# Performance work log

Measured on AMD Instinct MI355X. Metric: run time of the kernel, lower is better.

The kernel has to match this reference:

```python
import jax, jax.numpy as jnp
import numpy as np

KERNEL_SIZE = 5
SIGMA = 1.0
DARK_KS = 15


def _gaussian_kernel():
    x = jnp.arange(KERNEL_SIZE, dtype=jnp.float32) - KERNEL_SIZE // 2
    phi = jnp.exp(-0.5 * x * x / (SIGMA ** 2))
    phi = phi / (phi.sum() + 0.001)
    k2d = jnp.outer(phi, phi)                       # [5,5]
    return jnp.tile(k2d[None, None], (3, 1, 1, 1))  # [3,1,5,5] OIHW depthwise


def _tanh01(v):
    return jnp.tanh(v) * 0.5 + 0.5


def setup_inputs() -> dict:
    key = jax.random.key(0)
    k1, k2, k3 = jax.random.split(key, 3)
    # keep x strictly positive so x**param has well-defined gradients
    x = jax.random.uniform(k1, (16, 3, 512, 512), dtype=jnp.float32, minval=0.01, maxval=1.0)
    output1 = jax.random.normal(k2, (16, 7), dtype=jnp.float32)
    output2 = jax.random.normal(k3, (16, 4), dtype=jnp.float32)
    return {"x": x, "output1": output1, "output2": output2}


def reference(x, output1, output2):
    N, C, H, W = x.shape

    # ---- parameter squashing (clip_range + softmax weights) ----
    o1 = jnp.concatenate([
        _tanh01(output1[:, 0:1]) * 0.25 + 1.0,   # gamma param in [1, 1.25]
        _tanh01(output1[:, 1:2]) * 0.9 + 0.1,    # contrast alpha (dead branch)
        _tanh01(output1[:, 2:3]) * 2.0,          # sharpen lamda in [0, 2]
        _tanh01(output1[:, 3:4]),                # dehaze w in [0, 1]
        _tanh01(output1[:, 4:7]) * 0.1 + 0.95,   # WB gains in [0.95, 1.05]
    ], axis=1)
    o2 = jax.nn.softmax(_tanh01(output2), axis=1)  # [N,4] branch weights

    param = o1[:, 0][:, None, None, None]
    lamda = o1[:, 2][:, None, None, None]
    w = o1[:, 3][:, None, None, None]
    wb_params = o1[:, 4:7][:, :, None, None]

    # ---- WB ----
    x1 = jnp.clip(x * wb_params, 0.0, 1.0)

    # ---- GAMMA ----
    x2 = jnp.clip(x ** param + 0.001, 0.0, 1.0)

    # ---- SHARPEN (depthwise 5x5 gaussian blur, unsharp mask) ----
    gk = _gaussian_kernel()
    blur = jax.lax.conv_general_dilated(
        x, gk, window_strides=(1, 1), padding=((2, 2), (2, 2)),
        feature_group_count=3,
        dimension_numbers=("NCHW", "OIHW", "NCHW"))
    blur = jnp.clip(blur, 0.0, 1.0)
    x4 = jnp.clip(x + lamda * (x - blur), 0.0, 1.0)

    # ---- DEHAZE ----
    minc = jnp.min(x, axis=1, keepdims=True)  # [N,1,H,W]
    # avg_pool2d k=15 s=1 p=7 with count_include_pad=True -> sum window / 225
    dark = jax.lax.reduce_window(
        minc, 0.0, jax.lax.add, (1, 1, DARK_KS, DARK_KS), (1, 1, 1, 1),
        padding=[(0, 0), (0, 0), (DARK_KS // 2, DARK_KS // 2), (DARK_KS // 2, DARK_KS // 2)]
    ) / float(DARK_KS * DARK_KS)
    top_k = int(H * W * 0.05)
    flat_dark = dark.reshape(N, -1)
    _, top_idx = jax.lax.top_k(flat_dark, top_k)            # [N, top_k]
    flat_img = x.reshape(N, C, -1)
    sel = jnp.take_along_axis(flat_img, top_idx[:, None, :], axis=2)  # [N,C,top_k]
    A = sel.mean(axis=2)[:, :, None, None]                  # atmospheric light
    trans = 1.0 - w * dark
    trans = jnp.where(trans > 0.1, trans, jnp.float32(0.1))
    x5 = jnp.clip((x - A) / (trans + 0.001) + A, 0.0, 1.0)

    # ---- weighted combination (contrast branch is computed but unused upstream) ----
    w0 = o2[:, 0][:, None, None, None]
    w1 = o2[:, 1][:, None, None, None]
    w2 = o2[:, 2][:, None, None, None]
    w3 = o2[:, 3][:, None, None, None]
    x_sum = x + 0.1 * (w0 * x1 + w1 * x2 + w2 * x4 + w3 * x5)
    x_sum = x_sum / (jnp.sum(o2, axis=1)[:, None, None, None] + 0.001)

    # ---- per-sample per-channel min-max normalization ----
    min_vals = jnp.min(x_sum, axis=(2, 3), keepdims=True)
    max_vals = jnp.max(x_sum, axis=(2, 3), keepdims=True)
    return (x_sum - min_vals) / (max_vals - min_vals + 1e-07)
```

## Files before the change

### kernel.cpp

```cpp
#include <hip/hip_runtime.h>
#include <math.h>

#define NS   16
#define HH   512
#define WW   512
#define HW   (HH*WW)
#define TOPK 13107
#define NBIN 4096

#define O_O1   0
#define O_O2   112
#define O_DEN  176
#define O_KN   304
#define O_MMP  512
#define O_PART 25088
#define O_DARK 33280


#define G0 0.054466787f
#define G1 0.244103071f
#define G2 0.402457854f

__device__ __forceinline__ float tanh01(float v) { return tanhf(v)*0.5f + 0.5f; }
__device__ __forceinline__ float clamp01(float v) { return fminf(fmaxf(v, 0.0f), 1.0f); }
__device__ __forceinline__ int dark_bin(float v) {
  int b = (int)(v * (float)NBIN);
  return b > (NBIN-1) ? (NBIN-1) : (b < 0 ? 0 : b);
}

__global__ void k_zero(unsigned* __restrict__ hist) {
  int i = blockIdx.x * 256 + threadIdx.x;
  uint4 z; z.x = 0u; z.y = 0u; z.z = 0u; z.w = 0u;
  ((uint4*)hist)[i] = z;
}

__global__ void __launch_bounds__(256)
k_dark(const float* __restrict__ x, float* __restrict__ wsf, unsigned* __restrict__ hist) {
  __shared__ __align__(16) float sm[4096 + 46*64];
  float* minc = sm;
  unsigned* lh = (unsigned*)sm;
  float* hsum = sm + 4096;
  int tid = threadIdx.x;
  int w0 = blockIdx.x * 64, h0 = blockIdx.y * 32, n = blockIdx.z;
  const float* xb = x + (size_t)n*3*HW;

  for (int i = tid; i < 46*20; i += 256) {
    int r = i / 20, q = i - r*20;
    int hm = h0 - 7 + r, wc = w0 - 8 + 4*q;
    float4 v; v.x = 0.f; v.y = 0.f; v.z = 0.f; v.w = 0.f;
    if (hm >= 0 && hm < HH && wc >= 0 && wc < WW) {
      size_t o = (size_t)hm*WW + wc;
      float4 a = *(const float4*)&xb[o];
      float4 b = *(const float4*)&xb[HW + o];
      float4 c = *(const float4*)&xb[2*HW + o];
      v.x = fminf(fminf(a.x,b.x),c.x); v.y = fminf(fminf(a.y,b.y),c.y);
      v.z = fminf(fminf(a.z,b.z),c.z); v.w = fminf(fminf(a.w,b.w),c.w);
    }
    *(float4*)&minc[r*80 + 4*q] = v;
  }
  __syncthreads();
  for (int i = tid; i < 46*16; i += 256) {
    int r = i >> 4, c4 = (i & 15) * 4;
    const float4* mr = (const float4*)&minc[r*80];
    int qb = c4 >> 2;
    float m[20];
    #pragma unroll
    for (int t = 0; t < 5; ++t) {
      float4 v = mr[qb + t];
      m[4*t] = v.x; m[4*t+1] = v.y; m[4*t+2] = v.z; m[4*t+3] = v.w;
    }
    float s = 0.f;
    #pragma unroll
    for (int j = 1; j <= 15; ++j) s += m[j];
    float4 o;
    o.x = s; s += m[16] - m[1];
    o.y = s; s += m[17] - m[2];
    o.z = s; s += m[18] - m[3];
    o.w = s;
    *(float4*)&hsum[r*64 + c4] = o;
  }
  __syncthreads();
  for (int i = tid; i < NBIN; i += 256) lh[i] = 0u;
  __syncthreads();
  {
    int c = tid & 63, ty = tid >> 6, r0 = ty * 8;
    float s = 0.f;
    #pragma unroll
    for (int j = 0; j < 15; ++j) s += hsum[(r0 + j)*64 + c];
    float* dk = wsf + O_DARK + (size_t)n*HW;
    #pragma unroll
    for (int i = 0; i < 8; ++i) {
      int r = r0 + i;
      float v = s * (1.0f/225.0f);
      dk[(size_t)(h0 + r)*WW + w0 + c] = v;
      atomicAdd(&lh[dark_bin(v)], 1u);
      if (i < 7) s += hsum[(r + 15)*64 + c] - hsum[r*64 + c];
    }
  }
  __syncthreads();
  unsigned* gh = hist + n*NBIN;
  for (int i = tid; i < NBIN; i += 256) { unsigned v = lh[i]; if (v) atomicAdd(&gh[i], v); }
}

__global__ void __launch_bounds__(256)
k_asum(const float* __restrict__ x, float* __restrict__ wsf,
       const unsigned* __restrict__ hist, unsigned* __restrict__ wsu,
       const float* __restrict__ o1, const float* __restrict__ o2) {
  __shared__ __align__(16) unsigned lh[NBIN];
  __shared__ unsigned spp[256];
  __shared__ int sh_bsel;
  __shared__ float bl[4][7];
  int tid = threadIdx.x;
  int n = blockIdx.x >> 6, chunk = blockIdx.x & 63;
  const uint4* gh4 = (const uint4*)(hist + n*NBIN);
  unsigned ps = 0;
  #pragma unroll
  for (int k = 0; k < 4; ++k) {
    uint4 v = gh4[tid*4 + k];
    *(uint4*)&lh[tid*16 + 4*k] = v;
    ps += v.x + v.y + v.z + v.w;
  }
  spp[tid] = ps;
  __syncthreads();
  if (tid == 0) {
    const unsigned K = TOPK;
    unsigned cum = 0; int bsel = 0;
    for (int t = 255; t >= 0; --t) {
      if (cum + spp[t] >= K) {
        bsel = t*16;
        for (int b = t*16 + 15; b >= t*16; --b) {
          if (cum + lh[b] >= K) { bsel = b; break; }
          cum += lh[b];
        }
        break;
      }
      cum += spp[t];
    }
    sh_bsel = bsel;
    if (chunk == 0) {
      wsu[O_KN + n] = K - cum;
      wsf[O_O1+n*7+0] = tanh01(o1[n*7+0])*0.25f + 1.0f;
      wsf[O_O1+n*7+1] = tanh01(o1[n*7+1])*0.9f  + 0.1f;
      wsf[O_O1+n*7+2] = tanh01(o1[n*7+2])*2.0f;
      wsf[O_O1+n*7+3] = tanh01(o1[n*7+3]);
      wsf[O_O1+n*7+4] = tanh01(o1[n*7+4])*0.1f + 0.95f;
      wsf[O_O1+n*7+5] = tanh01(o1[n*7+5])*0.1f + 0.95f;
      wsf[O_O1+n*7+6] = tanh01(o1[n*7+6])*0.1f + 0.95f;
      float q0 = expf(tanh01(o2[n*4+0]));
      float q1 = expf(tanh01(o2[n*4+1]));
      float q2 = expf(tanh01(o2[n*4+2]));
      float q3 = expf(tanh01(o2[n*4+3]));
      float s = q0+q1+q2+q3;
      q0 /= s; q1 /= s; q2 /= s; q3 /= s;
      wsf[O_O2+n*4+0]=q0; wsf[O_O2+n*4+1]=q1; wsf[O_O2+n*4+2]=q2; wsf[O_O2+n*4+3]=q3;
      wsf[O_DEN+n] = (q0+q1+q2+q3) + 0.001f;
    }
  }
  __syncthreads();
  int bsel = sh_bsel;
  const float4* db = (const float4*)(wsf + O_DARK + (size_t)n*HW + (size_t)chunk*4096);
  const float4* x0 = (const float4*)(x + (size_t)n*3*HW + (size_t)chunk*4096);
  const float4* x1 = x0 + HW/4;
  const float4* x2 = x0 + HW/2;
  float s0=0,s1=0,s2=0,e0=0,e1=0,e2=0,ec=0;
  #pragma unroll
  for (int k = 0; k < 4; ++k) {
    int idx = k*256 + tid;
    float4 d = db[idx], a = x0[idx], b = x1[idx], c = x2[idx];
    #define ACC(DX, AX, BX, CX) { \
      int bb = dark_bin(DX); \
      bool gt = (bb > bsel), eq = (bb == bsel); \
      s0 += gt ? AX : 0.f; s1 += gt ? BX : 0.f; s2 += gt ? CX : 0.f; \
      e0 += eq ? AX : 0.f; e1 += eq ? BX : 0.f; e2 += eq ? CX : 0.f; \
      ec += eq ? 1.f : 0.f; }
    ACC(d.x, a.x, b.x, c.x) ACC(d.y, a.y, b.y, c.y)
    ACC(d.z, a.z, b.z, c.z) ACC(d.w, a.w, b.w, c.w)
    #undef ACC
  }
  #pragma unroll
  for (int off = 32; off; off >>= 1) {
    s0 += __shfl_down(s0, off); s1 += __shfl_down(s1, off); s2 += __shfl_down(s2, off);
    e0 += __shfl_down(e0, off); e1 += __shfl_down(e1, off); e2 += __shfl_down(e2, off);
    ec += __shfl_down(ec, off);
  }
  int wave = tid >> 6, lane = tid & 63;
  if (lane == 0) {
    bl[wave][0]=s0; bl[wave][1]=s1; bl[wave][2]=s2;
    bl[wave][3]=e0; bl[wave][4]=e1; bl[wave][5]=e2; bl[wave][6]=ec;
  }
  __syncthreads();
  if (tid < 7) wsf[O_PART + blockIdx.x*8 + tid] =
      bl[0][tid] + bl[1][tid] + bl[2][tid] + bl[3][tid];
}

__global__ void __launch_bounds__(256)
k_main(const float* __restrict__ x, float* __restrict__ wsf,
       const unsigned* __restrict__ wsu, float* __restrict__ out) {
  __shared__ __align__(16) float xs[20*72];
  __shared__ __align__(16) float hb[20*64];
  __shared__ float rmn[4], rmx[4];
  __shared__ float shA;
  int tid = threadIdx.x;
  int w0 = blockIdx.x * 64, h0 = blockIdx.y * 16;
  int z = blockIdx.z, n = z / 3, c = z % 3;
  const float* xc = x + (size_t)z*HW;
  for (int i = tid; i < 360; i += 256) {
    int r = i / 18, q = i - r*18;
    int gh = h0 - 2 + r, gw = w0 - 4 + 4*q;
    float4 v; v.x = 0.f; v.y = 0.f; v.z = 0.f; v.w = 0.f;
    if (gh >= 0 && gh < HH && gw >= 0 && gw < WW)
      v = *(const float4*)&xc[(size_t)gh*WW + gw];
    *(float4*)&xs[r*72 + 4*q] = v;
  }
  if (tid < 64) {
    const float* p = wsf + O_PART + (size_t)(n*64 + tid)*8;
    float sc_ = p[c], ec_ = p[3 + c], cc_ = p[6];
    #pragma unroll
    for (int off = 32; off; off >>= 1) {
      sc_ += __shfl_down(sc_, off);
      ec_ += __shfl_down(ec_, off);
      cc_ += __shfl_down(cc_, off);
    }
    if (tid == 0) {
      float kn = (float)wsu[O_KN + n];
      float ce = fmaxf(cc_, 1.0f);
      shA = (sc_ + kn * (ec_ / ce)) * (1.0f/(float)TOPK);
    }
  }
  __syncthreads();
  for (int i = tid; i < 320; i += 256) {
    int r = i >> 4, c4 = (i & 15) * 4;
    const float4* xr = (const float4*)&xs[r*72];
    int qb = c4 >> 2;
    float4 A4 = xr[qb], B4 = xr[qb+1], C4 = xr[qb+2];
    float m2=A4.z, m3=A4.w, m4=B4.x, m5=B4.y, m6=B4.z, m7=B4.w, m8=C4.x, m9=C4.y;
    float4 o;
    o.x = G0*(m2+m6) + G1*(m3+m5) + G2*m4;
    o.y = G0*(m3+m7) + G1*(m4+m6) + G2*m5;
    o.z = G0*(m4+m8) + G1*(m5+m7) + G2*m6;
    o.w = G0*(m5+m9) + G1*(m6+m8) + G2*m7;
    *(float4*)&hb[r*64 + c4] = o;
  }
  __syncthreads();
  float param = wsf[O_O1 + n*7 + 0];
  float lamda = wsf[O_O1 + n*7 + 2];
  float wpar  = wsf[O_O1 + n*7 + 3];
  float wb    = wsf[O_O1 + n*7 + 4 + c];
  float q0 = wsf[O_O2 + n*4 + 0], q1 = wsf[O_O2 + n*4 + 1];
  float q2 = wsf[O_O2 + n*4 + 2], q3 = wsf[O_O2 + n*4 + 3];
  float rden = 1.0f / wsf[O_DEN + n];
  float A = shA;
  int r = tid >> 4, c4 = (tid & 15) * 4;
  float4 xv = *(const float4*)&xs[(r+2)*72 + c4 + 4];
  float4 b0 = *(const float4*)&hb[(r+0)*64 + c4];
  float4 b1 = *(const float4*)&hb[(r+1)*64 + c4];
  float4 b2 = *(const float4*)&hb[(r+2)*64 + c4];
  float4 b3 = *(const float4*)&hb[(r+3)*64 + c4];
  float4 b4 = *(const float4*)&hb[(r+4)*64 + c4];
  const float* dark = wsf + O_DARK + (size_t)n*HW;
  float4 dk = *(const float4*)&dark[(size_t)(h0+r)*WW + w0 + c4];
  float4 osum;
  float mnv = 3.4e38f, mxv = -3.4e38f;
  #define PIX(OX, XV, B0, B1, B2, B3, B4, DK) { \
    float blur = clamp01(G0*(B0+B4) + G1*(B1+B3) + G2*B2); \
    float x4v = clamp01(XV + lamda*(XV - blur)); \
    float x1v = clamp01(XV * wb); \
    float x2v = clamp01(__expf(param*__logf(XV)) + 0.001f); \
    float tr = 1.0f - wpar*DK; tr = tr > 0.1f ? tr : 0.1f; \
    float x5v = clamp01((XV - A) * __builtin_amdgcn_rcpf(tr + 0.001f) + A); \
    OX = (XV + 0.1f*(q0*x1v + q1*x2v + q2*x4v + q3*x5v)) * rden; \
    mnv = fminf(mnv, OX); mxv = fmaxf(mxv, OX); }
  PIX(osum.x, xv.x, b0.x, b1.x, b2.x, b3.x, b4.x, dk.x)
  PIX(osum.y, xv.y, b0.y, b1.y, b2.y, b3.y, b4.y, dk.y)
  PIX(osum.z, xv.z, b0.z, b1.z, b2.z, b3.z, b4.z, dk.z)
  PIX(osum.w, xv.w, b0.w, b1.w, b2.w, b3.w, b4.w, dk.w)
  #undef PIX
  *(float4*)&out[(size_t)z*HW + (size_t)(h0+r)*WW + w0 + c4] = osum;
  #pragma unroll
  for (int off = 32; off; off >>= 1) {
    mnv = fminf(mnv, __shfl_down(mnv, off));
    mxv = fmaxf(mxv, __shfl_down(mxv, off));
  }
  int wave = tid >> 6, lane = tid & 63;
  if (lane == 0) { rmn[wave] = mnv; rmx[wave] = mxv; }
  __syncthreads();
  if (tid == 0) {
    mnv = fminf(fminf(rmn[0], rmn[1]), fminf(rmn[2], rmn[3]));
    mxv = fmaxf(fmaxf(rmx[0], rmx[1]), fmaxf(rmx[2], rmx[3]));
    int bxy = blockIdx.y * 8 + blockIdx.x;
    wsf[O_MMP + z*512 + bxy]       = mnv;
    wsf[O_MMP + z*512 + 256 + bxy] = mxv;
  }
}

__global__ void __launch_bounds__(256)
k_norm(float* __restrict__ out, const float* __restrict__ wsf) {
  __shared__ float rmn[4], rmx[4];
  int tid = threadIdx.x;
  int nc = blockIdx.x >> 5;
  int sub = blockIdx.x & 31;
  float mn = wsf[O_MMP + nc*512 + tid];
  float mx = wsf[O_MMP + nc*512 + 256 + tid];
  #pragma unroll
  for (int off = 32; off; off >>= 1) {
    mn = fminf(mn, __shfl_down(mn, off));
    mx = fmaxf(mx, __shfl_down(mx, off));
  }
  int wave = tid >> 6, lane = tid & 63;
  if (lane == 0) { rmn[wave] = mn; rmx[wave] = mx; }
  __syncthreads();
  mn = fminf(fminf(rmn[0], rmn[1]), fminf(rmn[2], rmn[3]));
  mx = fmaxf(fmaxf(rmx[0], rmx[1]), fmaxf(rmx[2], rmx[3]));
  float sc = 1.0f / (mx - mn + 1e-7f);
  float4* o4 = (float4*)out + (size_t)nc*65536 + (size_t)sub*2048;
  #pragma unroll
  for (int k = 0; k < 8; ++k) {
    float4 v = o4[k*256 + tid];
    v.x = (v.x - mn) * sc; v.y = (v.y - mn) * sc;
    v.z = (v.z - mn) * sc; v.w = (v.w - mn) * sc;
    o4[k*256 + tid] = v;
  }
}

extern "C" void kernel_launch(void* const* d_in, const int* in_sizes, int n_in,
                              void* d_out, int out_size, void* d_ws, size_t ws_size,
                              hipStream_t stream) {
  const float* x  = (const float*)d_in[0];
  const float* o1 = (const float*)d_in[1];
  const float* o2 = (const float*)d_in[2];
  float* out = (float*)d_out;
  float* wsf = (float*)d_ws;
  unsigned* wsu = (unsigned*)d_ws;
  unsigned* hist = (unsigned*)(out + (size_t)16*HW);

  k_zero<<<dim3(64), dim3(256), 0, stream>>>(hist);
  k_dark<<<dim3(8, 16, 16), dim3(256), 0, stream>>>(x, wsf, hist);
  k_asum<<<dim3(1024), dim3(256), 0, stream>>>(x, wsf, hist, wsu, o1, o2);
  k_main<<<dim3(8, 32, 48), dim3(256), 0, stream>>>(x, wsf, wsu, out);
  k_norm<<<dim3(1536), dim3(256), 0, stream>>>(out, wsf);
}
```

Before: 186.9 us.

## Accumulate per-bin channel sums in dark kernel, drop second full pass for atmospheric light

The dark-channel histogram now stores, per bin, a count plus the sums of the three input channels. A tiny per-sample kernel then finds the threshold bin and computes the atmospheric light from the bin sums. This removes the separate kernel that re-read the whole dark map and input. The main kernel now loops over the three channels inside one block, so the dark map is read once per pixel, and interior tiles skip bounds checks. In exchange there are many more shared and global float atomics, and a coarser 1024-bin histogram that approximates the tie bin by its mean.

```diff
diff --git a/kernel.cpp b/kernel.cpp
--- a/kernel.cpp
+++ b/kernel.cpp
@@ -6,14 +6,13 @@
 #define WW   512
 #define HW   (HH*WW)
 #define TOPK 13107
-#define NBIN 4096
+#define NBIN 1024
 
 #define O_O1   0
 #define O_O2   112
 #define O_DEN  176
-#define O_KN   304
+#define O_A    320
 #define O_MMP  512
-#define O_PART 25088
 #define O_DARK 33280
 
 
@@ -36,27 +35,43 @@
 
 __global__ void __launch_bounds__(256)
 k_dark(const float* __restrict__ x, float* __restrict__ wsf, unsigned* __restrict__ hist) {
-  __shared__ __align__(16) float sm[4096 + 46*64];
+  __shared__ __align__(16) float sm[7040];
   float* minc = sm;
-  unsigned* lh = (unsigned*)sm;
+  unsigned* bins = (unsigned*)sm;
+  float* binsf = sm;
   float* hsum = sm + 4096;
   int tid = threadIdx.x;
   int w0 = blockIdx.x * 64, h0 = blockIdx.y * 32, n = blockIdx.z;
   const float* xb = x + (size_t)n*3*HW;
 
-  for (int i = tid; i < 46*20; i += 256) {
-    int r = i / 20, q = i - r*20;
-    int hm = h0 - 7 + r, wc = w0 - 8 + 4*q;
-    float4 v; v.x = 0.f; v.y = 0.f; v.z = 0.f; v.w = 0.f;
-    if (hm >= 0 && hm < HH && wc >= 0 && wc < WW) {
-      size_t o = (size_t)hm*WW + wc;
+  bool interior = (w0 >= 8) && (w0 + 72 <= WW) && (h0 >= 7) && (h0 + 39 <= HH);
+  if (interior) {
+    for (int i = tid; i < 46*20; i += 256) {
+      int r = i / 20, q = i - r*20;
+      size_t o = (size_t)(h0 - 7 + r)*WW + (w0 - 8 + 4*q);
       float4 a = *(const float4*)&xb[o];
       float4 b = *(const float4*)&xb[HW + o];
       float4 c = *(const float4*)&xb[2*HW + o];
+      float4 v;
       v.x = fminf(fminf(a.x,b.x),c.x); v.y = fminf(fminf(a.y,b.y),c.y);
       v.z = fminf(fminf(a.z,b.z),c.z); v.w = fminf(fminf(a.w,b.w),c.w);
-    }
-    *(float4*)&minc[r*80 + 4*q] = v;
+      *(float4*)&minc[r*80 + 4*q] = v;
+    }
+  } else {
+    for (int i = tid; i < 46*20; i += 256) {
+      int r = i / 20, q = i - r*20;
+      int hm = h0 - 7 + r, wc = w0 - 8 + 4*q;
+      float4 v; v.x = 0.f; v.y = 0.f; v.z = 0.f; v.w = 0.f;
+      if (hm >= 0 && hm < HH && wc >= 0 && wc < WW) {
+        size_t o = (size_t)hm*WW + wc;
+        float4 a = *(const float4*)&xb[o];
+        float4 b = *(const float4*)&xb[HW + o];
+        float4 c = *(const float4*)&xb[2*HW + o];
+        v.x = fminf(fminf(a.x,b.x),c.x); v.y = fminf(fminf(a.y,b.y),c.y);
+        v.z = fminf(fminf(a.z,b.z),c.z); v.w = fminf(fminf(a.w,b.w),c.w);
+      }
+      *(float4*)&minc[r*80 + 4*q] = v;
+    }
   }
   __syncthreads();
   for (int i = tid; i < 46*16; i += 256) {
@@ -80,7 +95,7 @@
     *(float4*)&hsum[r*64 + c4] = o;
   }
   __syncthreads();
-  for (int i = tid; i < NBIN; i += 256) lh[i] = 0u;
+  for (int i = tid; i < 4096; i += 256) bins[i] = 0u;
   __syncthreads();
   {
     int c = tid & 63, ty = tid >> 6, r0 = ty * 8;
@@ -91,205 +106,200 @@
     #pragma unroll
     for (int i = 0; i < 8; ++i) {
       int r = r0 + i;
+      size_t po = (size_t)(h0 + r)*WW + w0 + c;
       float v = s * (1.0f/225.0f);
-      dk[(size_t)(h0 + r)*WW + w0 + c] = v;
-      atomicAdd(&lh[dark_bin(v)], 1u);
+      dk[po] = v;
+      int b = dark_bin(v);
+      float x0v = xb[po], x1v = xb[HW + po], x2v = xb[2*HW + po];
+      atomicAdd(&bins[b*4], 1u);
+      atomicAdd(&binsf[b*4+1], x0v);
+      atomicAdd(&binsf[b*4+2], x1v);
+      atomicAdd(&binsf[b*4+3], x2v);
       if (i < 7) s += hsum[(r + 15)*64 + c] - hsum[r*64 + c];
     }
   }
   __syncthreads();
-  unsigned* gh = hist + n*NBIN;
-  for (int i = tid; i < NBIN; i += 256) { unsigned v = lh[i]; if (v) atomicAdd(&gh[i], v); }
+  unsigned* gh = hist + n*NBIN*4;
+  for (int b = tid; b < NBIN; b += 256) {
+    unsigned cnt = bins[b*4];
+    if (cnt) {
+      atomicAdd(&gh[b*4], cnt);
+      atomicAdd((float*)&gh[b*4+1], binsf[b*4+1]);
+      atomicAdd((float*)&gh[b*4+2], binsf[b*4+2]);
+      atomicAdd((float*)&gh[b*4+3], binsf[b*4+3]);
+    }
+  }
 }
 
 __global__ void __launch_bounds__(256)
-k_asum(const float* __restrict__ x, float* __restrict__ wsf,
-       const unsigned* __restrict__ hist, unsigned* __restrict__ wsu,
-       const float* __restrict__ o1, const float* __restrict__ o2) {
-  __shared__ __align__(16) unsigned lh[NBIN];
-  __shared__ unsigned spp[256];
-  __shared__ int sh_bsel;
-  __shared__ float bl[4][7];
-  int tid = threadIdx.x;
-  int n = blockIdx.x >> 6, chunk = blockIdx.x & 63;
-  const uint4* gh4 = (const uint4*)(hist + n*NBIN);
+k_sel(const unsigned* __restrict__ hist, float* __restrict__ wsf,
+      const float* __restrict__ o1, const float* __restrict__ o2) {
+  __shared__ float s0s[NBIN], s1s[NBIN], s2s[NBIN];
+  __shared__ unsigned cnts[NBIN];
+  __shared__ unsigned partial[256];
+  __shared__ int sh_bsel; __shared__ float sh_kn;
+  __shared__ float red[4][3];
+  int n = blockIdx.x, tid = threadIdx.x;
+  const uint4* g4 = (const uint4*)(hist + n*NBIN*4);
   unsigned ps = 0;
   #pragma unroll
   for (int k = 0; k < 4; ++k) {
-    uint4 v = gh4[tid*4 + k];
-    *(uint4*)&lh[tid*16 + 4*k] = v;
-    ps += v.x + v.y + v.z + v.w;
-  }
-  spp[tid] = ps;
+    int b = tid*4 + k;
+    uint4 v = g4[b];
+    cnts[b] = v.x;
+    s0s[b] = __uint_as_float(v.y);
+    s1s[b] = __uint_as_float(v.z);
+    s2s[b] = __uint_as_float(v.w);
+    ps += v.x;
+  }
+  partial[tid] = ps;
   __syncthreads();
   if (tid == 0) {
     const unsigned K = TOPK;
     unsigned cum = 0; int bsel = 0;
     for (int t = 255; t >= 0; --t) {
-      if (cum + spp[t] >= K) {
-        bsel = t*16;
-        for (int b = t*16 + 15; b >= t*16; --b) {
-          if (cum + lh[b] >= K) { bsel = b; break; }
-          cum += lh[b];
+      if (cum + partial[t] >= K) {
+        bsel = t*4;
+        for (int b = t*4 + 3; b >= t*4; --b) {
+          if (cum + cnts[b] >= K) { bsel = b; break; }
+          cum += cnts[b];
         }
         break;
       }
-      cum += spp[t];
-    }
-    sh_bsel = bsel;
-    if (chunk == 0) {
-      wsu[O_KN + n] = K - cum;
-      wsf[O_O1+n*7+0] = tanh01(o1[n*7+0])*0.25f + 1.0f;
-      wsf[O_O1+n*7+1] = tanh01(o1[n*7+1])*0.9f  + 0.1f;
-      wsf[O_O1+n*7+2] = tanh01(o1[n*7+2])*2.0f;
-      wsf[O_O1+n*7+3] = tanh01(o1[n*7+3]);
-      wsf[O_O1+n*7+4] = tanh01(o1[n*7+4])*0.1f + 0.95f;
-      wsf[O_O1+n*7+5] = tanh01(o1[n*7+5])*0.1f + 0.95f;
-      wsf[O_O1+n*7+6] = tanh01(o1[n*7+6])*0.1f + 0.95f;
-      float q0 = expf(tanh01(o2[n*4+0]));
-      float q1 = expf(tanh01(o2[n*4+1]));
-      float q2 = expf(tanh01(o2[n*4+2]));
-      float q3 = expf(tanh01(o2[n*4+3]));
-      float s = q0+q1+q2+q3;
-      q0 /= s; q1 /= s; q2 /= s; q3 /= s;
-      wsf[O_O2+n*4+0]=q0; wsf[O_O2+n*4+1]=q1; wsf[O_O2+n*4+2]=q2; wsf[O_O2+n*4+3]=q3;
-      wsf[O_DEN+n] = (q0+q1+q2+q3) + 0.001f;
-    }
+      cum += partial[t];
+    }
+    sh_bsel = bsel; sh_kn = (float)(K - cum);
   }
   __syncthreads();
   int bsel = sh_bsel;
-  const float4* db = (const float4*)(wsf + O_DARK + (size_t)n*HW + (size_t)chunk*4096);
-  const float4* x0 = (const float4*)(x + (size_t)n*3*HW + (size_t)chunk*4096);
-  const float4* x1 = x0 + HW/4;
-  const float4* x2 = x0 + HW/2;
-  float s0=0,s1=0,s2=0,e0=0,e1=0,e2=0,ec=0;
-  #pragma unroll
-  for (int k = 0; k < 4; ++k) {
-    int idx = k*256 + tid;
-    float4 d = db[idx], a = x0[idx], b = x1[idx], c = x2[idx];
-    #define ACC(DX, AX, BX, CX) { \
-      int bb = dark_bin(DX); \
-      bool gt = (bb > bsel), eq = (bb == bsel); \
-      s0 += gt ? AX : 0.f; s1 += gt ? BX : 0.f; s2 += gt ? CX : 0.f; \
-      e0 += eq ? AX : 0.f; e1 += eq ? BX : 0.f; e2 += eq ? CX : 0.f; \
-      ec += eq ? 1.f : 0.f; }
-    ACC(d.x, a.x, b.x, c.x) ACC(d.y, a.y, b.y, c.y)
-    ACC(d.z, a.z, b.z, c.z) ACC(d.w, a.w, b.w, c.w)
-    #undef ACC
-  }
+  float a0 = 0.f, a1 = 0.f, a2 = 0.f;
+  for (int b = tid; b < NBIN; b += 256)
+    if (b > bsel) { a0 += s0s[b]; a1 += s1s[b]; a2 += s2s[b]; }
   #pragma unroll
   for (int off = 32; off; off >>= 1) {
-    s0 += __shfl_down(s0, off); s1 += __shfl_down(s1, off); s2 += __shfl_down(s2, off);
-    e0 += __shfl_down(e0, off); e1 += __shfl_down(e1, off); e2 += __shfl_down(e2, off);
-    ec += __shfl_down(ec, off);
+    a0 += __shfl_down(a0, off); a1 += __shfl_down(a1, off); a2 += __shfl_down(a2, off);
   }
   int wave = tid >> 6, lane = tid & 63;
-  if (lane == 0) {
-    bl[wave][0]=s0; bl[wave][1]=s1; bl[wave][2]=s2;
-    bl[wave][3]=e0; bl[wave][4]=e1; bl[wave][5]=e2; bl[wave][6]=ec;
-  }
-  __syncthreads();
-  if (tid < 7) wsf[O_PART + blockIdx.x*8 + tid] =
-      bl[0][tid] + bl[1][tid] + bl[2][tid] + bl[3][tid];
+  if (lane == 0) { red[wave][0] = a0; red[wave][1] = a1; red[wave][2] = a2; }
+  __syncthreads();
+  if (tid == 0) {
+    a0 = red[0][0]+red[1][0]+red[2][0]+red[3][0];
+    a1 = red[0][1]+red[1][1]+red[2][1]+red[3][1];
+    a2 = red[0][2]+red[1][2]+red[2][2]+red[3][2];
+    float kn = sh_kn;
+    float ce = fmaxf((float)cnts[bsel], 1.0f);
+    wsf[O_A + n*3 + 0] = (a0 + kn*(s0s[bsel]/ce)) * (1.0f/(float)TOPK);
+    wsf[O_A + n*3 + 1] = (a1 + kn*(s1s[bsel]/ce)) * (1.0f/(float)TOPK);
+    wsf[O_A + n*3 + 2] = (a2 + kn*(s2s[bsel]/ce)) * (1.0f/(float)TOPK);
+    wsf[O_O1+n*7+0] = tanh01(o1[n*7+0])*0.25f + 1.0f;
+    wsf[O_O1+n*7+1] = tanh01(o1[n*7+1])*0.9f  + 0.1f;
+    wsf[O_O1+n*7+2] = tanh01(o1[n*7+2])*2.0f;
+    wsf[O_O1+n*7+3] = tanh01(o1[n*7+3]);
+    wsf[O_O1+n*7+4] = tanh01(o1[n*7+4])*0.1f + 0.95f;
+    wsf[O_O1+n*7+5] = tanh01(o1[n*7+5])*0.1f + 0.95f;
+    wsf[O_O1+n*7+6] = tanh01(o1[n*7+6])*0.1f + 0.95f;
+    float q0 = expf(tanh01(o2[n*4+0]));
+    float q1 = expf(tanh01(o2[n*4+1]));
+    float q2 = expf(tanh01(o2[n*4+2]));
+    float q3 = expf(tanh01(o2[n*4+3]));
+    float s = q0+q1+q2+q3;
+    q0 /= s; q1 /= s; q2 /= s; q3 /= s;
+    wsf[O_O2+n*4+0]=q0; wsf[O_O2+n*4+1]=q1; wsf[O_O2+n*4+2]=q2; wsf[O_O2+n*4+3]=q3;
+    wsf[O_DEN+n] = (q0+q1+q2+q3) + 0.001f;
+  }
 }
 
 __global__ void __launch_bounds__(256)
-k_main(const float* __restrict__ x, float* __restrict__ wsf,
-       const unsigned* __restrict__ wsu, float* __restrict__ out) {
+k_main(const float* __restrict__ x, float* __restrict__ wsf, float* __restrict__ out) {
   __shared__ __align__(16) float xs[20*72];
   __shared__ __align__(16) float hb[20*64];
   __shared__ float rmn[4], rmx[4];
-  __shared__ float shA;
   int tid = threadIdx.x;
-  int w0 = blockIdx.x * 64, h0 = blockIdx.y * 16;
-  int z = blockIdx.z, n = z / 3, c = z % 3;
-  const float* xc = x + (size_t)z*HW;
-  for (int i = tid; i < 360; i += 256) {
-    int r = i / 18, q = i - r*18;
-    int gh = h0 - 2 + r, gw = w0 - 4 + 4*q;
-    float4 v; v.x = 0.f; v.y = 0.f; v.z = 0.f; v.w = 0.f;
-    if (gh >= 0 && gh < HH && gw >= 0 && gw < WW)
-      v = *(const float4*)&xc[(size_t)gh*WW + gw];
-    *(float4*)&xs[r*72 + 4*q] = v;
-  }
-  if (tid < 64) {
-    const float* p = wsf + O_PART + (size_t)(n*64 + tid)*8;
-    float sc_ = p[c], ec_ = p[3 + c], cc_ = p[6];
-    #pragma unroll
-    for (int off = 32; off; off >>= 1) {
-      sc_ += __shfl_down(sc_, off);
-      ec_ += __shfl_down(ec_, off);
-      cc_ += __shfl_down(cc_, off);
-    }
-    if (tid == 0) {
-      float kn = (float)wsu[O_KN + n];
-      float ce = fmaxf(cc_, 1.0f);
-      shA = (sc_ + kn * (ec_ / ce)) * (1.0f/(float)TOPK);
-    }
-  }
-  __syncthreads();
-  for (int i = tid; i < 320; i += 256) {
-    int r = i >> 4, c4 = (i & 15) * 4;
-    const float4* xr = (const float4*)&xs[r*72];
-    int qb = c4 >> 2;
-    float4 A4 = xr[qb], B4 = xr[qb+1], C4 = xr[qb+2];
-    float m2=A4.z, m3=A4.w, m4=B4.x, m5=B4.y, m6=B4.z, m7=B4.w, m8=C4.x, m9=C4.y;
-    float4 o;
-    o.x = G0*(m2+m6) + G1*(m3+m5) + G2*m4;
-    o.y = G0*(m3+m7) + G1*(m4+m6) + G2*m5;
-    o.z = G0*(m4+m8) + G1*(m5+m7) + G2*m6;
-    o.w = G0*(m5+m9) + G1*(m6+m8) + G2*m7;
-    *(float4*)&hb[r*64 + c4] = o;
-  }
-  __syncthreads();
+  int w0 = blockIdx.x * 64, h0 = blockIdx.y * 16, n = blockIdx.z;
+  int r = tid >> 4, c4 = (tid & 15) * 4;
+  int wave = tid >> 6, lane = tid & 63;
+  int bxy = blockIdx.y * 8 + blockIdx.x;
+  float4 dk = *(const float4*)&wsf[O_DARK + (size_t)n*HW + (size_t)(h0+r)*WW + w0 + c4];
   float param = wsf[O_O1 + n*7 + 0];
   float lamda = wsf[O_O1 + n*7 + 2];
   float wpar  = wsf[O_O1 + n*7 + 3];
-  float wb    = wsf[O_O1 + n*7 + 4 + c];
   float q0 = wsf[O_O2 + n*4 + 0], q1 = wsf[O_O2 + n*4 + 1];
   float q2 = wsf[O_O2 + n*4 + 2], q3 = wsf[O_O2 + n*4 + 3];
   float rden = 1.0f / wsf[O_DEN + n];
-  float A = shA;
-  int r = tid >> 4, c4 = (tid & 15) * 4;
-  float4 xv = *(const float4*)&xs[(r+2)*72 + c4 + 4];
-  float4 b0 = *(const float4*)&hb[(r+0)*64 + c4];
-  float4 b1 = *(const float4*)&hb[(r+1)*64 + c4];
-  float4 b2 = *(const float4*)&hb[(r+2)*64 + c4];
-  float4 b3 = *(const float4*)&hb[(r+3)*64 + c4];
-  float4 b4 = *(const float4*)&hb[(r+4)*64 + c4];
-  const float* dark = wsf + O_DARK + (size_t)n*HW;
-  float4 dk = *(const float4*)&dark[(size_t)(h0+r)*WW + w0 + c4];
-  float4 osum;
-  float mnv = 3.4e38f, mxv = -3.4e38f;
-  #define PIX(OX, XV, B0, B1, B2, B3, B4, DK) { \
-    float blur = clamp01(G0*(B0+B4) + G1*(B1+B3) + G2*B2); \
-    float x4v = clamp01(XV + lamda*(XV - blur)); \
-    float x1v = clamp01(XV * wb); \
-    float x2v = clamp01(__expf(param*__logf(XV)) + 0.001f); \
-    float tr = 1.0f - wpar*DK; tr = tr > 0.1f ? tr : 0.1f; \
-    float x5v = clamp01((XV - A) * __builtin_amdgcn_rcpf(tr + 0.001f) + A); \
-    OX = (XV + 0.1f*(q0*x1v + q1*x2v + q2*x4v + q3*x5v)) * rden; \
-    mnv = fminf(mnv, OX); mxv = fmaxf(mxv, OX); }
-  PIX(osum.x, xv.x, b0.x, b1.x, b2.x, b3.x, b4.x, dk.x)
-  PIX(osum.y, xv.y, b0.y, b1.y, b2.y, b3.y, b4.y, dk.y)
-  PIX(osum.z, xv.z, b0.z, b1.z, b2.z, b3.z, b4.z, dk.z)
-  PIX(osum.w, xv.w, b0.w, b1.w, b2.w, b3.w, b4.w, dk.w)
-  #undef PIX
-  *(float4*)&out[(size_t)z*HW + (size_t)(h0+r)*WW + w0 + c4] = osum;
-  #pragma unroll
-  for (int off = 32; off; off >>= 1) {
-    mnv = fminf(mnv, __shfl_down(mnv, off));
-    mxv = fmaxf(mxv, __shfl_down(mxv, off));
-  }
-  int wave = tid >> 6, lane = tid & 63;
-  if (lane == 0) { rmn[wave] = mnv; rmx[wave] = mxv; }
-  __syncthreads();
-  if (tid == 0) {
-    mnv = fminf(fminf(rmn[0], rmn[1]), fminf(rmn[2], rmn[3]));
-    mxv = fmaxf(fmaxf(rmx[0], rmx[1]), fmaxf(rmx[2], rmx[3]));
-    int bxy = blockIdx.y * 8 + blockIdx.x;
-    wsf[O_MMP + z*512 + bxy]       = mnv;
-    wsf[O_MMP + z*512 + 256 + bxy] = mxv;
+  bool interior = (w0 >= 4) && (w0 + 68 <= WW) && (h0 >= 2) && (h0 + 18 <= HH);
+
+  for (int c = 0; c < 3; ++c) {
+    int z = n*3 + c;
+    const float* xc = x + (size_t)z*HW;
+    if (interior) {
+      for (int i = tid; i < 360; i += 256) {
+        int rr = i / 18, q = i - rr*18;
+        *(float4*)&xs[rr*72 + 4*q] =
+            *(const float4*)&xc[(size_t)(h0 - 2 + rr)*WW + (w0 - 4 + 4*q)];
+      }
+    } else {
+      for (int i = tid; i < 360; i += 256) {
+        int rr = i / 18, q = i - rr*18;
+        int gh = h0 - 2 + rr, gw = w0 - 4 + 4*q;
+        float4 v; v.x = 0.f; v.y = 0.f; v.z = 0.f; v.w = 0.f;
+        if (gh >= 0 && gh < HH && gw >= 0 && gw < WW)
+          v = *(const float4*)&xc[(size_t)gh*WW + gw];
+        *(float4*)&xs[rr*72 + 4*q] = v;
+      }
+    }
+    __syncthreads();
+    for (int i = tid; i < 320; i += 256) {
+      int rr = i >> 4, cc4 = (i & 15) * 4;
+      const float4* xr = (const float4*)&xs[rr*72];
+      int qb = cc4 >> 2;
+      float4 A4 = xr[qb], B4 = xr[qb+1], C4 = xr[qb+2];
+      float m2=A4.z, m3=A4.w, m4=B4.x, m5=B4.y, m6=B4.z, m7=B4.w, m8=C4.x, m9=C4.y;
+      float4 o;
+      o.x = G0*(m2+m6) + G1*(m3+m5) + G2*m4;
+      o.y = G0*(m3+m7) + G1*(m4+m6) + G2*m5;
+      o.z = G0*(m4+m8) + G1*(m5+m7) + G2*m6;
+      o.w = G0*(m5+m9) + G1*(m6+m8) + G2*m7;
+      *(float4*)&hb[rr*64 + cc4] = o;
+    }
+    __syncthreads();
+    float wb = wsf[O_O1 + n*7 + 4 + c];
+    float A  = wsf[O_A + n*3 + c];
+    float4 xv = *(const float4*)&xs[(r+2)*72 + c4 + 4];
+    float4 b0 = *(const float4*)&hb[(r+0)*64 + c4];
+    float4 b1 = *(const float4*)&hb[(r+1)*64 + c4];
+    float4 b2 = *(const float4*)&hb[(r+2)*64 + c4];
+    float4 b3 = *(const float4*)&hb[(r+3)*64 + c4];
+    float4 b4 = *(const float4*)&hb[(r+4)*64 + c4];
+    float4 osum;
+    float mnv = 3.4e38f, mxv = -3.4e38f;
+    #define PIX(OX, XV, B0, B1, B2, B3, B4, DK) { \
+      float blur = clamp01(G0*(B0+B4) + G1*(B1+B3) + G2*B2); \
+      float x4v = clamp01(XV + lamda*(XV - blur)); \
+      float x1v = clamp01(XV * wb); \
+      float x2v = clamp01(__expf(param*__logf(XV)) + 0.001f); \
+      float tr = 1.0f - wpar*DK; tr = tr > 0.1f ? tr : 0.1f; \
+      float x5v = clamp01((XV - A) * __builtin_amdgcn_rcpf(tr + 0.001f) + A); \
+      OX = (XV + 0.1f*(q0*x1v + q1*x2v + q2*x4v + q3*x5v)) * rden; \
+      mnv = fminf(mnv, OX); mxv = fmaxf(mxv, OX); }
+    PIX(osum.x, xv.x, b0.x, b1.x, b2.x, b3.x, b4.x, dk.x)
+    PIX(osum.y, xv.y, b0.y, b1.y, b2.y, b3.y, b4.y, dk.y)
+    PIX(osum.z, xv.z, b0.z, b1.z, b2.z, b3.z, b4.z, dk.z)
+    PIX(osum.w, xv.w, b0.w, b1.w, b2.w, b3.w, b4.w, dk.w)
+    #undef PIX
+    *(float4*)&out[(size_t)z*HW + (size_t)(h0+r)*WW + w0 + c4] = osum;
+    #pragma unroll
+    for (int off = 32; off; off >>= 1) {
+      mnv = fminf(mnv, __shfl_down(mnv, off));
+      mxv = fmaxf(mxv, __shfl_down(mxv, off));
+    }
+    if (lane == 0) { rmn[wave] = mnv; rmx[wave] = mxv; }
+    __syncthreads();
+    if (tid == 0) {
+      mnv = fminf(fminf(rmn[0], rmn[1]), fminf(rmn[2], rmn[3]));
+      mxv = fmaxf(fmaxf(rmx[0], rmx[1]), fmaxf(rmx[2], rmx[3]));
+      wsf[O_MMP + z*512 + bxy]       = mnv;
+      wsf[O_MMP + z*512 + 256 + bxy] = mxv;
+    }
   }
 }
 
@@ -330,12 +340,11 @@
   const float* o2 = (const float*)d_in[2];
   float* out = (float*)d_out;
   float* wsf = (float*)d_ws;
-  unsigned* wsu = (unsigned*)d_ws;
   unsigned* hist = (unsigned*)(out + (size_t)16*HW);
 
   k_zero<<<dim3(64), dim3(256), 0, stream>>>(hist);
   k_dark<<<dim3(8, 16, 16), dim3(256), 0, stream>>>(x, wsf, hist);
-  k_asum<<<dim3(1024), dim3(256), 0, stream>>>(x, wsf, hist, wsu, o1, o2);
-  k_main<<<dim3(8, 32, 48), dim3(256), 0, stream>>>(x, wsf, wsu, out);
+  k_sel<<<dim3(16), dim3(256), 0, stream>>>(hist, wsf, o1, o2);
+  k_main<<<dim3(8, 32, 16), dim3(256), 0, stream>>>(x, wsf, out);
   k_norm<<<dim3(1536), dim3(256), 0, stream>>>(out, wsf);
 }
```

After: 262.9 us. +40.6%, slower.

## Process all three channels per k_main block and add interior fast paths

Applied to the files above, without the earlier changes.

k_main now loops over the three channels inside each block instead of launching one block per channel. The dark-channel tile, the per-sample parameters and the atmospheric-light reduction are loaded or computed once per block, which cuts redundant global reads of the dark map and the partial sums. Both k_dark and k_main get a branch-free tile-loading path for blocks away from the image border. In exchange there are three times fewer blocks, each doing serial per-channel work with more barriers, so there is less parallelism to hide latency.

```diff
diff --git a/kernel.cpp b/kernel.cpp
--- a/kernel.cpp
+++ b/kernel.cpp
@@ -44,19 +44,34 @@
   int w0 = blockIdx.x * 64, h0 = blockIdx.y * 32, n = blockIdx.z;
   const float* xb = x + (size_t)n*3*HW;
 
-  for (int i = tid; i < 46*20; i += 256) {
-    int r = i / 20, q = i - r*20;
-    int hm = h0 - 7 + r, wc = w0 - 8 + 4*q;
-    float4 v; v.x = 0.f; v.y = 0.f; v.z = 0.f; v.w = 0.f;
-    if (hm >= 0 && hm < HH && wc >= 0 && wc < WW) {
-      size_t o = (size_t)hm*WW + wc;
+  bool interior = (w0 >= 8) && (w0 + 72 <= WW) && (h0 >= 7) && (h0 + 39 <= HH);
+  if (interior) {
+    for (int i = tid; i < 46*20; i += 256) {
+      int r = i / 20, q = i - r*20;
+      size_t o = (size_t)(h0 - 7 + r)*WW + (w0 - 8 + 4*q);
       float4 a = *(const float4*)&xb[o];
       float4 b = *(const float4*)&xb[HW + o];
       float4 c = *(const float4*)&xb[2*HW + o];
+      float4 v;
       v.x = fminf(fminf(a.x,b.x),c.x); v.y = fminf(fminf(a.y,b.y),c.y);
       v.z = fminf(fminf(a.z,b.z),c.z); v.w = fminf(fminf(a.w,b.w),c.w);
-    }
-    *(float4*)&minc[r*80 + 4*q] = v;
+      *(float4*)&minc[r*80 + 4*q] = v;
+    }
+  } else {
+    for (int i = tid; i < 46*20; i += 256) {
+      int r = i / 20, q = i - r*20;
+      int hm = h0 - 7 + r, wc = w0 - 8 + 4*q;
+      float4 v; v.x = 0.f; v.y = 0.f; v.z = 0.f; v.w = 0.f;
+      if (hm >= 0 && hm < HH && wc >= 0 && wc < WW) {
+        size_t o = (size_t)hm*WW + wc;
+        float4 a = *(const float4*)&xb[o];
+        float4 b = *(const float4*)&xb[HW + o];
+        float4 c = *(const float4*)&xb[2*HW + o];
+        v.x = fminf(fminf(a.x,b.x),c.x); v.y = fminf(fminf(a.y,b.y),c.y);
+        v.z = fminf(fminf(a.z,b.z),c.z); v.w = fminf(fminf(a.w,b.w),c.w);
+      }
+      *(float4*)&minc[r*80 + 4*q] = v;
+    }
   }
   __syncthreads();
   for (int i = tid; i < 46*16; i += 256) {
@@ -199,97 +214,110 @@
   __shared__ __align__(16) float xs[20*72];
   __shared__ __align__(16) float hb[20*64];
   __shared__ float rmn[4], rmx[4];
-  __shared__ float shA;
+  __shared__ float shA[3];
   int tid = threadIdx.x;
-  int w0 = blockIdx.x * 64, h0 = blockIdx.y * 16;
-  int z = blockIdx.z, n = z / 3, c = z % 3;
-  const float* xc = x + (size_t)z*HW;
-  for (int i = tid; i < 360; i += 256) {
-    int r = i / 18, q = i - r*18;
-    int gh = h0 - 2 + r, gw = w0 - 4 + 4*q;
-    float4 v; v.x = 0.f; v.y = 0.f; v.z = 0.f; v.w = 0.f;
-    if (gh >= 0 && gh < HH && gw >= 0 && gw < WW)
-      v = *(const float4*)&xc[(size_t)gh*WW + gw];
-    *(float4*)&xs[r*72 + 4*q] = v;
-  }
-  if (tid < 64) {
-    const float* p = wsf + O_PART + (size_t)(n*64 + tid)*8;
-    float sc_ = p[c], ec_ = p[3 + c], cc_ = p[6];
-    #pragma unroll
-    for (int off = 32; off; off >>= 1) {
-      sc_ += __shfl_down(sc_, off);
-      ec_ += __shfl_down(ec_, off);
-      cc_ += __shfl_down(cc_, off);
-    }
-    if (tid == 0) {
-      float kn = (float)wsu[O_KN + n];
-      float ce = fmaxf(cc_, 1.0f);
-      shA = (sc_ + kn * (ec_ / ce)) * (1.0f/(float)TOPK);
-    }
-  }
-  __syncthreads();
-  for (int i = tid; i < 320; i += 256) {
-    int r = i >> 4, c4 = (i & 15) * 4;
-    const float4* xr = (const float4*)&xs[r*72];
-    int qb = c4 >> 2;
-    float4 A4 = xr[qb], B4 = xr[qb+1], C4 = xr[qb+2];
-    float m2=A4.z, m3=A4.w, m4=B4.x, m5=B4.y, m6=B4.z, m7=B4.w, m8=C4.x, m9=C4.y;
-    float4 o;
-    o.x = G0*(m2+m6) + G1*(m3+m5) + G2*m4;
-    o.y = G0*(m3+m7) + G1*(m4+m6) + G2*m5;
-    o.z = G0*(m4+m8) + G1*(m5+m7) + G2*m6;
-    o.w = G0*(m5+m9) + G1*(m6+m8) + G2*m7;
-    *(float4*)&hb[r*64 + c4] = o;
-  }
-  __syncthreads();
+  int w0 = blockIdx.x * 64, h0 = blockIdx.y * 16, n = blockIdx.z;
+  int r = tid >> 4, c4 = (tid & 15) * 4;
+  int wave = tid >> 6, lane = tid & 63;
+  int bxy = blockIdx.y * 8 + blockIdx.x;
+  float4 dk = *(const float4*)&wsf[O_DARK + (size_t)n*HW + (size_t)(h0+r)*WW + w0 + c4];
   float param = wsf[O_O1 + n*7 + 0];
   float lamda = wsf[O_O1 + n*7 + 2];
   float wpar  = wsf[O_O1 + n*7 + 3];
-  float wb    = wsf[O_O1 + n*7 + 4 + c];
   float q0 = wsf[O_O2 + n*4 + 0], q1 = wsf[O_O2 + n*4 + 1];
   float q2 = wsf[O_O2 + n*4 + 2], q3 = wsf[O_O2 + n*4 + 3];
   float rden = 1.0f / wsf[O_DEN + n];
-  float A = shA;
-  int r = tid >> 4, c4 = (tid & 15) * 4;
-  float4 xv = *(const float4*)&xs[(r+2)*72 + c4 + 4];
-  float4 b0 = *(const float4*)&hb[(r+0)*64 + c4];
-  float4 b1 = *(const float4*)&hb[(r+1)*64 + c4];
-  float4 b2 = *(const float4*)&hb[(r+2)*64 + c4];
-  float4 b3 = *(const float4*)&hb[(r+3)*64 + c4];
-  float4 b4 = *(const float4*)&hb[(r+4)*64 + c4];
-  const float* dark = wsf + O_DARK + (size_t)n*HW;
-  float4 dk = *(const float4*)&dark[(size_t)(h0+r)*WW + w0 + c4];
-  float4 osum;
-  float mnv = 3.4e38f, mxv = -3.4e38f;
-  #define PIX(OX, XV, B0, B1, B2, B3, B4, DK) { \
-    float blur = clamp01(G0*(B0+B4) + G1*(B1+B3) + G2*B2); \
-    float x4v = clamp01(XV + lamda*(XV - blur)); \
-    float x1v = clamp01(XV * wb); \
-    float x2v = clamp01(__expf(param*__logf(XV)) + 0.001f); \
-    float tr = 1.0f - wpar*DK; tr = tr > 0.1f ? tr : 0.1f; \
-    float x5v = clamp01((XV - A) * __builtin_amdgcn_rcpf(tr + 0.001f) + A); \
-    OX = (XV + 0.1f*(q0*x1v + q1*x2v + q2*x4v + q3*x5v)) * rden; \
-    mnv = fminf(mnv, OX); mxv = fmaxf(mxv, OX); }
-  PIX(osum.x, xv.x, b0.x, b1.x, b2.x, b3.x, b4.x, dk.x)
-  PIX(osum.y, xv.y, b0.y, b1.y, b2.y, b3.y, b4.y, dk.y)
-  PIX(osum.z, xv.z, b0.z, b1.z, b2.z, b3.z, b4.z, dk.z)
-  PIX(osum.w, xv.w, b0.w, b1.w, b2.w, b3.w, b4.w, dk.w)
-  #undef PIX
-  *(float4*)&out[(size_t)z*HW + (size_t)(h0+r)*WW + w0 + c4] = osum;
-  #pragma unroll
-  for (int off = 32; off; off >>= 1) {
-    mnv = fminf(mnv, __shfl_down(mnv, off));
-    mxv = fmaxf(mxv, __shfl_down(mxv, off));
-  }
-  int wave = tid >> 6, lane = tid & 63;
-  if (lane == 0) { rmn[wave] = mnv; rmx[wave] = mxv; }
-  __syncthreads();
-  if (tid == 0) {
-    mnv = fminf(fminf(rmn[0], rmn[1]), fminf(rmn[2], rmn[3]));
-    mxv = fmaxf(fmaxf(rmx[0], rmx[1]), fmaxf(rmx[2], rmx[3]));
-    int bxy = blockIdx.y * 8 + blockIdx.x;
-    wsf[O_MMP + z*512 + bxy]       = mnv;
-    wsf[O_MMP + z*512 + 256 + bxy] = mxv;
+  bool interior = (w0 >= 4) && (w0 + 68 <= WW) && (h0 >= 2) && (h0 + 18 <= HH);
+  if (tid < 64) {
+    const float* p = wsf + O_PART + (size_t)(n*64 + tid)*8;
+    float s0=p[0], s1=p[1], s2=p[2], e0=p[3], e1=p[4], e2=p[5], ec=p[6];
+    #pragma unroll
+    for (int off = 32; off; off >>= 1) {
+      s0 += __shfl_down(s0, off); s1 += __shfl_down(s1, off); s2 += __shfl_down(s2, off);
+      e0 += __shfl_down(e0, off); e1 += __shfl_down(e1, off); e2 += __shfl_down(e2, off);
+      ec += __shfl_down(ec, off);
+    }
+    if (tid == 0) {
+      float kn = (float)wsu[O_KN + n];
+      float ce = fmaxf(ec, 1.0f);
+      shA[0] = (s0 + kn * (e0 / ce)) * (1.0f/(float)TOPK);
+      shA[1] = (s1 + kn * (e1 / ce)) * (1.0f/(float)TOPK);
+      shA[2] = (s2 + kn * (e2 / ce)) * (1.0f/(float)TOPK);
+    }
+  }
+
+  for (int c = 0; c < 3; ++c) {
+    int z = n*3 + c;
+    const float* xc = x + (size_t)z*HW;
+    if (interior) {
+      for (int i = tid; i < 360; i += 256) {
+        int rr = i / 18, q = i - rr*18;
+        *(float4*)&xs[rr*72 + 4*q] =
+            *(const float4*)&xc[(size_t)(h0 - 2 + rr)*WW + (w0 - 4 + 4*q)];
+      }
+    } else {
+      for (int i = tid; i < 360; i += 256) {
+        int rr = i / 18, q = i - rr*18;
+        int gh = h0 - 2 + rr, gw = w0 - 4 + 4*q;
+        float4 v; v.x = 0.f; v.y = 0.f; v.z = 0.f; v.w = 0.f;
+        if (gh >= 0 && gh < HH && gw >= 0 && gw < WW)
+          v = *(const float4*)&xc[(size_t)gh*WW + gw];
+        *(float4*)&xs[rr*72 + 4*q] = v;
+      }
+    }
+    __syncthreads();
+    for (int i = tid; i < 320; i += 256) {
+      int rr = i >> 4, cc4 = (i & 15) * 4;
+      const float4* xr = (const float4*)&xs[rr*72];
+      int qb = cc4 >> 2;
+      float4 A4 = xr[qb], B4 = xr[qb+1], C4 = xr[qb+2];
+      float m2=A4.z, m3=A4.w, m4=B4.x, m5=B4.y, m6=B4.z, m7=B4.w, m8=C4.x, m9=C4.y;
+      float4 o;
+      o.x = G0*(m2+m6) + G1*(m3+m5) + G2*m4;
+      o.y = G0*(m3+m7) + G1*(m4+m6) + G2*m5;
+      o.z = G0*(m4+m8) + G1*(m5+m7) + G2*m6;
+      o.w = G0*(m5+m9) + G1*(m6+m8) + G2*m7;
+      *(float4*)&hb[rr*64 + cc4] = o;
+    }
+    __syncthreads();
+    float wb = wsf[O_O1 + n*7 + 4 + c];
+    float A  = shA[c];
+    float4 xv = *(const float4*)&xs[(r+2)*72 + c4 + 4];
+    float4 b0 = *(const float4*)&hb[(r+0)*64 + c4];
+    float4 b1 = *(const float4*)&hb[(r+1)*64 + c4];
+    float4 b2 = *(const float4*)&hb[(r+2)*64 + c4];
+    float4 b3 = *(const float4*)&hb[(r+3)*64 + c4];
+    float4 b4 = *(const float4*)&hb[(r+4)*64 + c4];
+    float4 osum;
+    float mnv = 3.4e38f, mxv = -3.4e38f;
+    #define PIX(OX, XV, B0, B1, B2, B3, B4, DK) { \
+      float blur = clamp01(G0*(B0+B4) + G1*(B1+B3) + G2*B2); \
+      float x4v = clamp01(XV + lamda*(XV - blur)); \
+      float x1v = clamp01(XV * wb); \
+      float x2v = clamp01(__expf(param*__logf(XV)) + 0.001f); \
+      float tr = 1.0f - wpar*DK; tr = tr > 0.1f ? tr : 0.1f; \
+      float x5v = clamp01((XV - A) * __builtin_amdgcn_rcpf(tr + 0.001f) + A); \
+      OX = (XV + 0.1f*(q0*x1v + q1*x2v + q2*x4v + q3*x5v)) * rden; \
+      mnv = fminf(mnv, OX); mxv = fmaxf(mxv, OX); }
+    PIX(osum.x, xv.x, b0.x, b1.x, b2.x, b3.x, b4.x, dk.x)
+    PIX(osum.y, xv.y, b0.y, b1.y, b2.y, b3.y, b4.y, dk.y)
+    PIX(osum.z, xv.z, b0.z, b1.z, b2.z, b3.z, b4.z, dk.z)
+    PIX(osum.w, xv.w, b0.w, b1.w, b2.w, b3.w, b4.w, dk.w)
+    #undef PIX
+    *(float4*)&out[(size_t)z*HW + (size_t)(h0+r)*WW + w0 + c4] = osum;
+    #pragma unroll
+    for (int off = 32; off; off >>= 1) {
+      mnv = fminf(mnv, __shfl_down(mnv, off));
+      mxv = fmaxf(mxv, __shfl_down(mxv, off));
+    }
+    if (lane == 0) { rmn[wave] = mnv; rmx[wave] = mxv; }
+    __syncthreads();
+    if (tid == 0) {
+      mnv = fminf(fminf(rmn[0], rmn[1]), fminf(rmn[2], rmn[3]));
+      mxv = fmaxf(fmaxf(rmx[0], rmx[1]), fmaxf(rmx[2], rmx[3]));
+      wsf[O_MMP + z*512 + bxy]       = mnv;
+      wsf[O_MMP + z*512 + 256 + bxy] = mxv;
+    }
   }
 }
 
@@ -336,6 +364,6 @@
   k_zero<<<dim3(64), dim3(256), 0, stream>>>(hist);
   k_dark<<<dim3(8, 16, 16), dim3(256), 0, stream>>>(x, wsf, hist);
   k_asum<<<dim3(1024), dim3(256), 0, stream>>>(x, wsf, hist, wsu, o1, o2);
-  k_main<<<dim3(8, 32, 48), dim3(256), 0, stream>>>(x, wsf, wsu, out);
+  k_main<<<dim3(8, 32, 16), dim3(256), 0, stream>>>(x, wsf, wsu, out);
   k_norm<<<dim3(1536), dim3(256), 0, stream>>>(out, wsf);
 }
```

Result: no change. 186.8 us (-0.1%).
